# Kernel optimization log

Measured on AMD Instinct MI355X. Metric: run time of the kernel, lower is better.

Reference implementation:

```python
import jax, jax.numpy as jnp
import numpy as np

N = 8192
F_IN = 256
F_OUT = 128
NEG = -9.0e15

def setup_inputs() -> dict:
    key = jax.random.key(0)
    k1, k2, k3, k4 = jax.random.split(key, 4)
    x = jax.random.normal(k1, (N, F_IN), dtype=jnp.float32)
    adj = jax.random.randint(k2, (N, N), 0, 2, dtype=jnp.int32)
    # xavier-uniform-ish scales
    W = jax.random.normal(k3, (F_IN, F_OUT), dtype=jnp.float32) * (1.414 / np.sqrt(F_IN))
    a = jax.random.normal(k4, (2 * F_OUT, 1), dtype=jnp.float32) * (1.414 / np.sqrt(F_OUT))
    return {"x": x, "adj": adj, "W": W, "a": a}

def reference(x, adj, W, a):
    # h_i = W^T x_i  -> [N, F_OUT]
    h = x @ W
    # torch builds atom_trans[i,j] = concat(h_i, h_j); e[i,j] = leakyrelu(a1.h_i + a2.h_j)
    a1 = a[:F_OUT, 0]   # [F_OUT]
    a2 = a[F_OUT:, 0]   # [F_OUT]
    s1 = h @ a1         # [N]
    s2 = h @ a2         # [N]
    e = jax.nn.leaky_relu(s1[:, None] + s2[None, :], negative_slope=0.01)  # [N, N]
    masked = jnp.where(adj > 0, e, jnp.full_like(e, NEG))
    attention = jax.nn.softmax(masked, axis=1)
    # dropout is identity in eval mode
    h1 = attention @ h  # [N, F_OUT]
    return jax.nn.elu(h1)
```

## Files before the change

### kernel.cpp

```cpp
#include <hip/hip_runtime.h>
#include <hip/hip_bf16.h>
#include <cstdint>
#include <cstddef>

#define NN 8192
#define FIN 256
#define FO 128
#define SPLITK 8
#define JCH 1024
#define NIT 16

typedef float f32x4 __attribute__((ext_vector_type(4)));
typedef _Float16 f16x8 __attribute__((ext_vector_type(8)));

typedef __attribute__((address_space(3))) void lds_void;
typedef const __attribute__((address_space(1))) void glb_void;
__device__ __forceinline__ void gl_lds16(const void* g, void* l) {
  __builtin_amdgcn_global_load_lds((glb_void*)g, (lds_void*)l, 16, 0, 0);
}

__device__ __forceinline__ unsigned enc_f32(float f) {
  unsigned u = __float_as_uint(f);
  return (u & 0x80000000u) ? ~u : (u | 0x80000000u);
}
__device__ __forceinline__ float dec_f32(unsigned u) {
  unsigned b = (u & 0x80000000u) ? (u ^ 0x80000000u) : ~u;
  return __uint_as_float(b);
}

__global__ void k1_xw(const float* __restrict__ x, const float* __restrict__ W,
                      float* __restrict__ h, unsigned* __restrict__ enc) {
  __shared__ float xs[32 * 66];
  __shared__ float Ws[64 * 128];
  int t = threadIdx.x;
  int r0 = blockIdx.x * 32;
  if (blockIdx.x == 0 && t == 0) *enc = 0u;
  int r = t & 31, cg = t >> 5;
  float acc[16];
#pragma unroll
  for (int i = 0; i < 16; ++i) acc[i] = 0.f;
  for (int ko = 0; ko < 4; ++ko) {
    __syncthreads();
    {
      int rr = t >> 3, kc = (t & 7) * 8;
      const float2* src = (const float2*)(x + (size_t)(r0 + rr) * FIN + ko * 64 + kc);
      float2* dst = (float2*)&xs[rr * 66 + kc];
#pragma unroll
      for (int q = 0; q < 4; ++q) dst[q] = src[q];
    }
    {
      int kk = t >> 2, q = t & 3;
      const float4* src = (const float4*)(W + (size_t)(ko * 64 + kk) * FO + q * 32);
      float4* dst = (float4*)&Ws[kk * 128 + q * 32];
#pragma unroll
      for (int i = 0; i < 8; ++i) dst[i] = src[i];
    }
    __syncthreads();
#pragma unroll 8
    for (int kk = 0; kk < 64; ++kk) {
      float xv = xs[r * 66 + kk];
      const float4* wr = (const float4*)&Ws[kk * 128 + cg * 16];
      float4 w0 = wr[0], w1 = wr[1], w2 = wr[2], w3 = wr[3];
      acc[0]  = fmaf(xv, w0.x, acc[0]);  acc[1]  = fmaf(xv, w0.y, acc[1]);
      acc[2]  = fmaf(xv, w0.z, acc[2]);  acc[3]  = fmaf(xv, w0.w, acc[3]);
      acc[4]  = fmaf(xv, w1.x, acc[4]);  acc[5]  = fmaf(xv, w1.y, acc[5]);
      acc[6]  = fmaf(xv, w1.z, acc[6]);  acc[7]  = fmaf(xv, w1.w, acc[7]);
      acc[8]  = fmaf(xv, w2.x, acc[8]);  acc[9]  = fmaf(xv, w2.y, acc[9]);
      acc[10] = fmaf(xv, w2.z, acc[10]); acc[11] = fmaf(xv, w2.w, acc[11]);
      acc[12] = fmaf(xv, w3.x, acc[12]); acc[13] = fmaf(xv, w3.y, acc[13]);
      acc[14] = fmaf(xv, w3.z, acc[14]); acc[15] = fmaf(xv, w3.w, acc[15]);
    }
  }
  float* hp = h + (size_t)(r0 + r) * FO + cg * 16;
#pragma unroll
  for (int i = 0; i < 4; ++i)
    ((float4*)hp)[i] = make_float4(acc[4 * i], acc[4 * i + 1], acc[4 * i + 2], acc[4 * i + 3]);
}

__global__ void k2_prep(const float* __restrict__ h, const float* __restrict__ a,
                        _Float16* __restrict__ hT,
                        float* __restrict__ s1, float* __restrict__ s2,
                        unsigned* __restrict__ enc) {
  __shared__ float ht[64 * 129];
  int t = threadIdx.x;
  int r0 = blockIdx.x * 64;
  {
    int rr = t >> 2, q = t & 3;
    const float4* src = (const float4*)(h + (size_t)(r0 + rr) * FO + q * 32);
    float* dst = &ht[rr * 129 + q * 32];
#pragma unroll
    for (int i = 0; i < 8; ++i) {
      float4 v = src[i];
      dst[4 * i + 0] = v.x; dst[4 * i + 1] = v.y;
      dst[4 * i + 2] = v.z; dst[4 * i + 3] = v.w;
    }
  }
  __syncthreads();
  {
    int c = t >> 1, half = t & 1;
    alignas(16) _Float16 buf[32];
#pragma unroll
    for (int i = 0; i < 32; ++i) buf[i] = (_Float16)ht[(half * 32 + i) * 129 + c];
    int4* d = (int4*)(hT + (size_t)c * NN + r0 + half * 32);
#pragma unroll
    for (int i = 0; i < 4; ++i) d[i] = ((const int4*)buf)[i];
  }
  if (t < 64) {
    int row = r0 + t;
    float v1 = 0.f, v2 = 0.f;
#pragma unroll 16
    for (int c = 0; c < FO; ++c) {
      float hv = ht[t * 129 + c];
      v1 = fmaf(hv, a[c], v1);
      v2 = fmaf(hv, a[FO + c], v2);
    }
    s1[row] = v1; s2[row] = v2;
    float m = v2;
#pragma unroll
    for (int off = 1; off < 64; off <<= 1) m = fmaxf(m, __shfl_xor(m, off));
    if (t == 0) atomicMax(enc, enc_f32(m));
  }
}

__device__ __forceinline__ _Float16 wel(unsigned av, float s2v, float s1v, float mv, float& sum) {
  float tt = s1v + s2v;
  tt = fmaxf(tt, 0.01f * tt);
  float wf = av ? __expf(tt - mv) : 0.f;
  _Float16 wh = (_Float16)wf;
  sum += (float)wh;
  return wh;
}

#define K4BODY(CR, NR, BUF, JC, PF, LAST)                                        \
  {                                                                              \
    if (PF) {                                                                    \
      stage(BUF ^ 1, (JC) + 64);                                                 \
      _Pragma("unroll")                                                          \
      for (int rr = 0; rr < 16; ++rr)                                            \
        NR[rr] = abase[(size_t)rr * NN + (JC) + 64];                             \
    }                                                                            \
    __builtin_amdgcn_sched_barrier(0);                                           \
    unsigned mlo = 0u, mhi = 0u;                                                 \
    _Pragma("unroll")                                                            \
    for (int rr = 0; rr < 16; ++rr) {                                            \
      unsigned long long br = __ballot(CR[rr] > 0);                              \
      bool sel = (l15 == rr);                                                    \
      mlo = sel ? (unsigned)br : mlo;                                            \
      mhi = sel ? (unsigned)(br >> 32) : mhi;                                    \
    }                                                                            \
    _Pragma("unroll")                                                            \
    for (int ks = 0; ks < 2; ++ks) {                                             \
      unsigned mm = ks ? mhi : mlo;                                              \
      unsigned byt = (mm >> (kgrp << 3)) & 0xffu;                                \
      int jloc = ((JC) - jbeg) + ks * 32 + kgrp * 8;                             \
      f32x4 sa = *(const f32x4*)&s2l[jloc];                                      \
      f32x4 sb = *(const f32x4*)&s2l[jloc + 4];                                  \
      f16x8 af;                                                                  \
      af[0] = wel(byt & 1u,   sa[0], s10, m0, sum0);                             \
      af[1] = wel(byt & 2u,   sa[1], s10, m0, sum0);                             \
      af[2] = wel(byt & 4u,   sa[2], s10, m0, sum0);                             \
      af[3] = wel(byt & 8u,   sa[3], s10, m0, sum0);                             \
      af[4] = wel(byt & 16u,  sb[0], s10, m0, sum0);                             \
      af[5] = wel(byt & 32u,  sb[1], s10, m0, sum0);                             \
      af[6] = wel(byt & 64u,  sb[2], s10, m0, sum0);                             \
      af[7] = wel(byt & 128u, sb[3], s10, m0, sum0);                             \
      _Pragma("unroll")                                                          \
      for (int cf = 0; cf < 8; ++cf) {                                           \
        f16x8 bfr = *(const f16x8*)&tile[BUF][(cf * 16 + l15) * 64 +             \
                       ((ks * 32 + kgrp * 8) ^ (l7 * 8))];                       \
        acc[cf] = __builtin_amdgcn_mfma_f32_16x16x32_f16(af, bfr, acc[cf], 0, 0, 0); \
      }                                                                          \
    }                                                                            \
    __builtin_amdgcn_sched_barrier(0);                                           \
    if (!(LAST)) {                                                               \
      asm volatile("s_waitcnt vmcnt(16)" ::: "memory");                          \
      __builtin_amdgcn_s_barrier();                                              \
      __builtin_amdgcn_sched_barrier(0);                                         \
    }                                                                            \
  }

__global__ void __launch_bounds__(256, 4) k4_main(
    const int* __restrict__ adj, const float* __restrict__ s1g,
    const float* __restrict__ s2g, const unsigned* __restrict__ enc,
    const _Float16* __restrict__ hT,
    float* __restrict__ num_p, float* __restrict__ den_p) {
  __shared__ _Float16 tile[2][128 * 64];
  __shared__ float s2l[JCH];
  int t = threadIdx.x;
  int l = t & 63, wv = t >> 6;
  int l15 = l & 15, kgrp = l >> 4;
  int l7 = l15 & 7;
  int split = blockIdx.x;
  int r0 = blockIdx.y * 64;
  int jbeg = split * JCH;
  int row = r0 + wv * 16 + l15;

  float c2 = dec_f32(*enc);
  float s10 = s1g[row];
  float m0 = s10 + c2; m0 = fmaxf(m0, 0.01f * m0);

  f32x4 acc[8];
#pragma unroll
  for (int cf = 0; cf < 8; ++cf) acc[cf] = (f32x4){0.f, 0.f, 0.f, 0.f};
  float sum0 = 0.f;
  const int* abase = adj + (size_t)(r0 + wv * 16) * NN + l;

  auto stage = [&](int b, int jg) {
    const _Float16* g0 = hT + (size_t)(wv * 32 + (l >> 3)) * NN + jg +
                         (((l & 7) ^ (l >> 3)) * 8);
    _Float16* base = &tile[b][(wv * 32) * 64];
    gl_lds16(g0, base);
    gl_lds16(g0 + (size_t)8 * NN, base + 8 * 64);
    gl_lds16(g0 + (size_t)16 * NN, base + 16 * 64);
    gl_lds16(g0 + (size_t)24 * NN, base + 24 * 64);
  };

  int ra[16], rb[16];
  stage(0, jbeg);
  *(float4*)&s2l[t * 4] = *(const float4*)(s2g + jbeg + t * 4);
#pragma unroll
  for (int rr = 0; rr < 16; ++rr) ra[rr] = abase[(size_t)rr * NN + jbeg];
  __syncthreads();

#pragma unroll 1
  for (int tI = 0; tI < NIT; tI += 2) {
    int jc = jbeg + tI * 64;
    K4BODY(ra, rb, 0, jc, true, false);
    K4BODY(rb, ra, 1, jc + 64, (tI + 2 < NIT), (tI + 2 >= NIT));
  }

  sum0 += __shfl_xor(sum0, 16);
  sum0 += __shfl_xor(sum0, 32);
  size_t sbase = (size_t)split * NN;
  if (l < 16) den_p[sbase + r0 + wv * 16 + l] = sum0;
#pragma unroll
  for (int cf = 0; cf < 8; ++cf) {
#pragma unroll
    for (int i = 0; i < 4; ++i) {
      int orow = r0 + wv * 16 + kgrp * 4 + i;
      int ocol = cf * 16 + l15;
      num_p[(sbase + orow) * (size_t)FO + ocol] = acc[cf][i];
    }
  }
}

__global__ void k5_fin(const float* __restrict__ num_p, const float* __restrict__ den_p,
                       float* __restrict__ out) {
  int idx = blockIdx.x * 256 + threadIdx.x;
  int row = idx >> 7;
  float num = 0.f, den = 0.f;
#pragma unroll
  for (int s = 0; s < SPLITK; ++s) {
    num += num_p[(size_t)s * (NN * FO) + idx];
    den += den_p[(size_t)s * NN + row];
  }
  float v = num / den;
  out[idx] = v > 0.f ? v : expm1f(v);
}

extern "C" void kernel_launch(void* const* d_in, const int* in_sizes, int n_in,
                              void* d_out, int out_size, void* d_ws, size_t ws_size,
                              hipStream_t stream) {
  const float* x   = (const float*)d_in[0];
  const int*   adj = (const int*)d_in[1];
  const float* W   = (const float*)d_in[2];
  const float* a   = (const float*)d_in[3];
  float* out = (float*)d_out;
  char* ws = (char*)d_ws;

  float*     h     = (float*)ws;
  _Float16*  hT    = (_Float16*)(ws + ((size_t)4 << 20));
  float*     s1    = (float*)(ws + ((size_t)6 << 20));
  float*     s2    = (float*)(ws + ((size_t)6 << 20) + (32u << 10));
  unsigned*  enc   = (unsigned*)(ws + ((size_t)6 << 20) + (64u << 10));
  float*     den_p = (float*)(ws + ((size_t)6 << 20) + (128u << 10));
  float*     num_p = (float*)(ws + ((size_t)7 << 20));

  k1_xw<<<dim3(256), dim3(256), 0, stream>>>(x, W, h, enc);
  k2_prep<<<dim3(128), dim3(256), 0, stream>>>(h, a, hT, s1, s2, enc);
  k4_main<<<dim3(SPLITK, 128), dim3(256), 0, stream>>>(adj, s1, s2, enc, hT,
                                                       num_p, den_p);
  k5_fin<<<dim3((NN * FO) / 256), dim3(256), 0, stream>>>(num_p, den_p, out);
}
```

Baseline: 114.9 us.

## Load adjacency as int2 pairs over 128-column superblocks with split even/odd ballots

Each lane now loads two adjacent adjacency ints (int2) per row, so one set of 16 loads covers 128 columns instead of 64. Ballots are split into even and odd masks, and the weight construction interleaves bits from the two masks. The main loop is restructured into superblocks of two 64-column MFMA phases, with hT staging and barriers rearranged. This halves the number of adjacency load instructions and ballot rounds per column. In exchange it adds scheduling complexity and different vmcnt accounting.

```diff
diff --git a/kernel.cpp b/kernel.cpp
--- a/kernel.cpp
+++ b/kernel.cpp
@@ -8,7 +8,7 @@
 #define FO 128
 #define SPLITK 8
 #define JCH 1024
-#define NIT 16
+#define NSB 8
 
 typedef float f32x4 __attribute__((ext_vector_type(4)));
 typedef _Float16 f16x8 __attribute__((ext_vector_type(8)));
@@ -131,51 +131,30 @@
   return wh;
 }
 
-#define K4BODY(CR, NR, BUF, JC, PF, LAST)                                        \
+#define K4COMPUTE(MEV, MOD, BUFI, SBASE)                                         \
   {                                                                              \
-    if (PF) {                                                                    \
-      stage(BUF ^ 1, (JC) + 64);                                                 \
-      _Pragma("unroll")                                                          \
-      for (int rr = 0; rr < 16; ++rr)                                            \
-        NR[rr] = abase[(size_t)rr * NN + (JC) + 64];                             \
-    }                                                                            \
-    __builtin_amdgcn_sched_barrier(0);                                           \
-    unsigned mlo = 0u, mhi = 0u;                                                 \
-    _Pragma("unroll")                                                            \
-    for (int rr = 0; rr < 16; ++rr) {                                            \
-      unsigned long long br = __ballot(CR[rr] > 0);                              \
-      bool sel = (l15 == rr);                                                    \
-      mlo = sel ? (unsigned)br : mlo;                                            \
-      mhi = sel ? (unsigned)(br >> 32) : mhi;                                    \
-    }                                                                            \
     _Pragma("unroll")                                                            \
     for (int ks = 0; ks < 2; ++ks) {                                             \
-      unsigned mm = ks ? mhi : mlo;                                              \
-      unsigned byt = (mm >> (kgrp << 3)) & 0xffu;                                \
-      int jloc = ((JC) - jbeg) + ks * 32 + kgrp * 8;                             \
+      unsigned ne = ((MEV) >> (ks * 16 + kgrp * 4)) & 0xfu;                      \
+      unsigned no = ((MOD) >> (ks * 16 + kgrp * 4)) & 0xfu;                      \
+      int jloc = (SBASE) + ks * 32 + kgrp * 8;                                   \
       f32x4 sa = *(const f32x4*)&s2l[jloc];                                      \
       f32x4 sb = *(const f32x4*)&s2l[jloc + 4];                                  \
       f16x8 af;                                                                  \
-      af[0] = wel(byt & 1u,   sa[0], s10, m0, sum0);                             \
-      af[1] = wel(byt & 2u,   sa[1], s10, m0, sum0);                             \
-      af[2] = wel(byt & 4u,   sa[2], s10, m0, sum0);                             \
-      af[3] = wel(byt & 8u,   sa[3], s10, m0, sum0);                             \
-      af[4] = wel(byt & 16u,  sb[0], s10, m0, sum0);                             \
-      af[5] = wel(byt & 32u,  sb[1], s10, m0, sum0);                             \
-      af[6] = wel(byt & 64u,  sb[2], s10, m0, sum0);                             \
-      af[7] = wel(byt & 128u, sb[3], s10, m0, sum0);                             \
+      af[0] = wel(ne & 1u, sa[0], s10, m0, sum0);                                \
+      af[1] = wel(no & 1u, sa[1], s10, m0, sum0);                                \
+      af[2] = wel(ne & 2u, sa[2], s10, m0, sum0);                                \
+      af[3] = wel(no & 2u, sa[3], s10, m0, sum0);                                \
+      af[4] = wel(ne & 4u, sb[0], s10, m0, sum0);                                \
+      af[5] = wel(no & 4u, sb[1], s10, m0, sum0);                                \
+      af[6] = wel(ne & 8u, sb[2], s10, m0, sum0);                                \
+      af[7] = wel(no & 8u, sb[3], s10, m0, sum0);                                \
       _Pragma("unroll")                                                          \
       for (int cf = 0; cf < 8; ++cf) {                                           \
-        f16x8 bfr = *(const f16x8*)&tile[BUF][(cf * 16 + l15) * 64 +             \
+        f16x8 bfr = *(const f16x8*)&tile[BUFI][(cf * 16 + l15) * 64 +            \
                        ((ks * 32 + kgrp * 8) ^ (l7 * 8))];                       \
         acc[cf] = __builtin_amdgcn_mfma_f32_16x16x32_f16(af, bfr, acc[cf], 0, 0, 0); \
       }                                                                          \
-    }                                                                            \
-    __builtin_amdgcn_sched_barrier(0);                                           \
-    if (!(LAST)) {                                                               \
-      asm volatile("s_waitcnt vmcnt(16)" ::: "memory");                          \
-      __builtin_amdgcn_s_barrier();                                              \
-      __builtin_amdgcn_sched_barrier(0);                                         \
     }                                                                            \
   }
 
@@ -203,7 +182,7 @@
 #pragma unroll
   for (int cf = 0; cf < 8; ++cf) acc[cf] = (f32x4){0.f, 0.f, 0.f, 0.f};
   float sum0 = 0.f;
-  const int* abase = adj + (size_t)(r0 + wv * 16) * NN + l;
+  const int* abase = adj + (size_t)(r0 + wv * 16) * NN + 2 * l;
 
   auto stage = [&](int b, int jg) {
     const _Float16* g0 = hT + (size_t)(wv * 32 + (l >> 3)) * NN + jg +
@@ -215,31 +194,72 @@
     gl_lds16(g0 + (size_t)24 * NN, base + 24 * 64);
   };
 
-  int ra[16], rb[16];
+  int2 S[16];
+#define LOADSET2(J)                                                              \
+  _Pragma("unroll")                                                              \
+  for (int rr = 0; rr < 16; ++rr)                                                \
+    S[rr] = *(const int2*)(abase + (size_t)rr * NN + (J));
+
+  unsigned mev_lo, mev_hi, mod_lo, mod_hi;
+#define BALLOTROUTE()                                                            \
+  {                                                                              \
+    mev_lo = 0u; mev_hi = 0u; mod_lo = 0u; mod_hi = 0u;                          \
+    _Pragma("unroll")                                                            \
+    for (int rr = 0; rr < 16; ++rr) {                                            \
+      unsigned long long be = __ballot(S[rr].x > 0);                             \
+      unsigned long long bo = __ballot(S[rr].y > 0);                             \
+      bool sel = (l15 == rr);                                                    \
+      mev_lo = sel ? (unsigned)be : mev_lo;                                      \
+      mev_hi = sel ? (unsigned)(be >> 32) : mev_hi;                              \
+      mod_lo = sel ? (unsigned)bo : mod_lo;                                      \
+      mod_hi = sel ? (unsigned)(bo >> 32) : mod_hi;                              \
+    }                                                                            \
+  }
+
   stage(0, jbeg);
+  LOADSET2(jbeg)
   *(float4*)&s2l[t * 4] = *(const float4*)(s2g + jbeg + t * 4);
-#pragma unroll
-  for (int rr = 0; rr < 16; ++rr) ra[rr] = abase[(size_t)rr * NN + jbeg];
-  __syncthreads();
+  asm volatile("s_waitcnt vmcnt(0) lgkmcnt(0)" ::: "memory");
+  __builtin_amdgcn_s_barrier();
+  __builtin_amdgcn_sched_barrier(0);
+  BALLOTROUTE()
 
 #pragma unroll 1
-  for (int tI = 0; tI < NIT; tI += 2) {
-    int jc = jbeg + tI * 64;
-    K4BODY(ra, rb, 0, jc, true, false);
-    K4BODY(rb, ra, 1, jc + 64, (tI + 2 < NIT), (tI + 2 >= NIT));
+  for (int sb = 0; sb < NSB; ++sb) {
+    int sjb = jbeg + sb * 128;
+    int sbase = sb * 128;
+    stage(1, sjb + 64);
+    if (sb + 1 < NSB) { LOADSET2(sjb + 128) }
+    __builtin_amdgcn_sched_barrier(0);
+    K4COMPUTE(mev_lo, mod_lo, 0, sbase)
+    __builtin_amdgcn_sched_barrier(0);
+    if (sb + 1 < NSB) asm volatile("s_waitcnt vmcnt(16)" ::: "memory");
+    else              asm volatile("s_waitcnt vmcnt(0)" ::: "memory");
+    __builtin_amdgcn_s_barrier();
+    __builtin_amdgcn_sched_barrier(0);
+    if (sb + 1 < NSB) stage(0, sjb + 128);
+    __builtin_amdgcn_sched_barrier(0);
+    K4COMPUTE(mev_hi, mod_hi, 1, sbase + 64)
+    __builtin_amdgcn_sched_barrier(0);
+    if (sb + 1 < NSB) {
+      asm volatile("s_waitcnt vmcnt(0)" ::: "memory");
+      __builtin_amdgcn_s_barrier();
+      __builtin_amdgcn_sched_barrier(0);
+      BALLOTROUTE()
+    }
   }
 
   sum0 += __shfl_xor(sum0, 16);
   sum0 += __shfl_xor(sum0, 32);
-  size_t sbase = (size_t)split * NN;
-  if (l < 16) den_p[sbase + r0 + wv * 16 + l] = sum0;
+  size_t sbase2 = (size_t)split * NN;
+  if (l < 16) den_p[sbase2 + r0 + wv * 16 + l] = sum0;
 #pragma unroll
   for (int cf = 0; cf < 8; ++cf) {
 #pragma unroll
     for (int i = 0; i < 4; ++i) {
       int orow = r0 + wv * 16 + kgrp * 4 + i;
       int ocol = cf * 16 + l15;
-      num_p[(sbase + orow) * (size_t)FO + ocol] = acc[cf][i];
+      num_p[(sbase2 + orow) * (size_t)FO + ocol] = acc[cf][i];
     }
   }
 }
```

After: 120.2 us. +4.6%, slower.

## Warp-specialize attention kernel with producer waves building adjacency bitmasks in LDS

Applied to the files above, without the earlier changes.

Adds two producer waves per block that load the int32 adjacency with 16-byte vector loads, ballot it into 64-bit masks and store them in shared memory. The four consumer waves stage h tiles and run the MFMA softmax-weighted accumulation, reading the precomputed masks. The aim is to take the adjacency loads and ballots off the MFMA waves' critical path and widen the adj loads. The cost is 384-thread blocks with lower occupancy, extra LDS for the masks, and a per-step barrier shared by both roles.

```diff
diff --git a/kernel.cpp b/kernel.cpp
--- a/kernel.cpp
+++ b/kernel.cpp
@@ -8,10 +8,10 @@
 #define FO 128
 #define SPLITK 8
 #define JCH 1024
-#define NIT 16
 
 typedef float f32x4 __attribute__((ext_vector_type(4)));
 typedef _Float16 f16x8 __attribute__((ext_vector_type(8)));
+typedef unsigned long long ull;
 
 typedef __attribute__((address_space(3))) void lds_void;
 typedef const __attribute__((address_space(1))) void glb_void;
@@ -131,79 +131,116 @@
   return wh;
 }
 
-#define K4BODY(CR, NR, BUF, JC, PF, LAST)                                        \
+#define PLOAD(SET, T)                                                            \
+  if ((T) < 8) {                                                                 \
+    int wl_ = ((T) >> 2) + 2, sub_ = (T) & 3;                                    \
+    const int* pb = adj + (size_t)(r0 + p32 + sub_ * 8) * NN + jbeg +            \
+                    wl_ * 256 + 4 * l;                                           \
+    _Pragma("unroll")                                                            \
+    for (int rr = 0; rr < 8; ++rr)                                               \
+      SET[rr] = *(const int4*)(pb + (size_t)rr * NN);                            \
+  }
+
+#define PBALLOT(SET, T)                                                          \
+  if ((T) >= 1 && (T) <= 8) {                                                    \
+    int wl_ = (((T) - 1) >> 2) + 2, sub_ = ((T) - 1) & 3;                        \
+    if ((T) < 8) asm volatile("s_waitcnt vmcnt(8)" ::: "memory");                \
+    else         asm volatile("s_waitcnt vmcnt(0)" ::: "memory");                \
+    _Pragma("unroll")                                                            \
+    for (int rr = 0; rr < 8; ++rr) {                                             \
+      ull b0 = __ballot(SET[rr].x > 0);                                          \
+      ull b1 = __ballot(SET[rr].y > 0);                                          \
+      ull b2 = __ballot(SET[rr].z > 0);                                          \
+      ull b3 = __ballot(SET[rr].w > 0);                                          \
+      if (l == 0) {                                                              \
+        int row_ = p32 + sub_ * 8 + rr;                                          \
+        masksL[row_][wl_ * 4 + 0] = b0;                                          \
+        masksL[row_][wl_ * 4 + 1] = b1;                                          \
+        masksL[row_][wl_ * 4 + 2] = b2;                                          \
+        masksL[row_][wl_ * 4 + 3] = b3;                                          \
+      }                                                                          \
+    }                                                                            \
+  }
+
+#define CONSUME(BUFI, T)                                                         \
   {                                                                              \
-    if (PF) {                                                                    \
-      stage(BUF ^ 1, (JC) + 64);                                                 \
-      _Pragma("unroll")                                                          \
-      for (int rr = 0; rr < 16; ++rr)                                            \
-        NR[rr] = abase[(size_t)rr * NN + (JC) + 64];                             \
-    }                                                                            \
-    __builtin_amdgcn_sched_barrier(0);                                           \
-    unsigned mlo = 0u, mhi = 0u;                                                 \
-    _Pragma("unroll")                                                            \
-    for (int rr = 0; rr < 16; ++rr) {                                            \
-      unsigned long long br = __ballot(CR[rr] > 0);                              \
-      bool sel = (l15 == rr);                                                    \
-      mlo = sel ? (unsigned)br : mlo;                                            \
-      mhi = sel ? (unsigned)(br >> 32) : mhi;                                    \
-    }                                                                            \
+    int win_ = (T) >> 2, sub_ = (T) & 3;                                         \
+    const ull* mrow = &masksL[(wv << 4) + l15][win_ << 2];                       \
+    ull w0 = mrow[0] >> sh2, w1 = mrow[1] >> sh2,                                \
+        w2 = mrow[2] >> sh2, w3 = mrow[3] >> sh2;                                \
     _Pragma("unroll")                                                            \
     for (int ks = 0; ks < 2; ++ks) {                                             \
-      unsigned mm = ks ? mhi : mlo;                                              \
-      unsigned byt = (mm >> (kgrp << 3)) & 0xffu;                                \
-      int jloc = ((JC) - jbeg) + ks * 32 + kgrp * 8;                             \
+      int SH = sub_ * 16 + ks * 8;                                               \
+      unsigned b0 = (unsigned)(w0 >> SH);                                        \
+      unsigned b1 = (unsigned)(w1 >> SH);                                        \
+      unsigned b2 = (unsigned)(w2 >> SH);                                        \
+      unsigned b3 = (unsigned)(w3 >> SH);                                        \
+      int jloc = (T) * 64 + ks * 32 + kgrp * 8;                                  \
       f32x4 sa = *(const f32x4*)&s2l[jloc];                                      \
       f32x4 sb = *(const f32x4*)&s2l[jloc + 4];                                  \
       f16x8 af;                                                                  \
-      af[0] = wel(byt & 1u,   sa[0], s10, m0, sum0);                             \
-      af[1] = wel(byt & 2u,   sa[1], s10, m0, sum0);                             \
-      af[2] = wel(byt & 4u,   sa[2], s10, m0, sum0);                             \
-      af[3] = wel(byt & 8u,   sa[3], s10, m0, sum0);                             \
-      af[4] = wel(byt & 16u,  sb[0], s10, m0, sum0);                             \
-      af[5] = wel(byt & 32u,  sb[1], s10, m0, sum0);                             \
-      af[6] = wel(byt & 64u,  sb[2], s10, m0, sum0);                             \
-      af[7] = wel(byt & 128u, sb[3], s10, m0, sum0);                             \
+      af[0] = wel(b0 & 1u, sa[0], s10, m0, sum0);                                \
+      af[1] = wel(b1 & 1u, sa[1], s10, m0, sum0);                                \
+      af[2] = wel(b2 & 1u, sa[2], s10, m0, sum0);                                \
+      af[3] = wel(b3 & 1u, sa[3], s10, m0, sum0);                                \
+      af[4] = wel(b0 & 2u, sb[0], s10, m0, sum0);                                \
+      af[5] = wel(b1 & 2u, sb[1], s10, m0, sum0);                                \
+      af[6] = wel(b2 & 2u, sb[2], s10, m0, sum0);                                \
+      af[7] = wel(b3 & 2u, sb[3], s10, m0, sum0);                                \
       _Pragma("unroll")                                                          \
       for (int cf = 0; cf < 8; ++cf) {                                           \
-        f16x8 bfr = *(const f16x8*)&tile[BUF][(cf * 16 + l15) * 64 +             \
+        f16x8 bfr = *(const f16x8*)&tile[(BUFI)][(cf * 16 + l15) * 64 +          \
                        ((ks * 32 + kgrp * 8) ^ (l7 * 8))];                       \
         acc[cf] = __builtin_amdgcn_mfma_f32_16x16x32_f16(af, bfr, acc[cf], 0, 0, 0); \
       }                                                                          \
     }                                                                            \
+  }
+
+#define BODYALL(T, LSET, BSET)                                                   \
+  {                                                                              \
+    if (wv < 4) {                                                                \
+      if ((T) < 15) stage(((T) + 1) & 1, jbeg + ((T) + 1) * 64);                 \
+      CONSUME((T) & 1, T)                                                        \
+    } else {                                                                     \
+      PLOAD(LSET, T)                                                             \
+      PBALLOT(BSET, T)                                                           \
+    }                                                                            \
     __builtin_amdgcn_sched_barrier(0);                                           \
-    if (!(LAST)) {                                                               \
-      asm volatile("s_waitcnt vmcnt(16)" ::: "memory");                          \
+    if ((T) < 15) {                                                              \
+      if (wv < 4) asm volatile("s_waitcnt vmcnt(0)" ::: "memory");               \
+      else        asm volatile("s_waitcnt lgkmcnt(0)" ::: "memory");             \
       __builtin_amdgcn_s_barrier();                                              \
       __builtin_amdgcn_sched_barrier(0);                                         \
     }                                                                            \
   }
 
-__global__ void __launch_bounds__(256, 4) k4_main(
+__global__ void __launch_bounds__(384, 3) k4_main(
     const int* __restrict__ adj, const float* __restrict__ s1g,
     const float* __restrict__ s2g, const unsigned* __restrict__ enc,
     const _Float16* __restrict__ hT,
     float* __restrict__ num_p, float* __restrict__ den_p) {
   __shared__ _Float16 tile[2][128 * 64];
   __shared__ float s2l[JCH];
+  __shared__ ull masksL[64][16];
   int t = threadIdx.x;
   int l = t & 63, wv = t >> 6;
   int l15 = l & 15, kgrp = l >> 4;
   int l7 = l15 & 7;
+  int sh2 = kgrp * 2;
   int split = blockIdx.x;
   int r0 = blockIdx.y * 64;
   int jbeg = split * JCH;
-  int row = r0 + wv * 16 + l15;
-
+  int p32 = (wv - 4) * 32;
+
+  int crow = r0 + (wv & 3) * 16 + l15;
   float c2 = dec_f32(*enc);
-  float s10 = s1g[row];
+  float s10 = s1g[crow];
   float m0 = s10 + c2; m0 = fmaxf(m0, 0.01f * m0);
 
   f32x4 acc[8];
 #pragma unroll
   for (int cf = 0; cf < 8; ++cf) acc[cf] = (f32x4){0.f, 0.f, 0.f, 0.f};
   float sum0 = 0.f;
-  const int* abase = adj + (size_t)(r0 + wv * 16) * NN + l;
 
   auto stage = [&](int b, int jg) {
     const _Float16* g0 = hT + (size_t)(wv * 32 + (l >> 3)) * NN + jg +
@@ -215,31 +252,62 @@
     gl_lds16(g0 + (size_t)24 * NN, base + 24 * 64);
   };
 
-  int ra[16], rb[16];
-  stage(0, jbeg);
-  *(float4*)&s2l[t * 4] = *(const float4*)(s2g + jbeg + t * 4);
-#pragma unroll
-  for (int rr = 0; rr < 16; ++rr) ra[rr] = abase[(size_t)rr * NN + jbeg];
-  __syncthreads();
-
+  int4 Sa[8], Sb[8];
+
+  if (wv < 4) {
+    stage(0, jbeg);
+    asm volatile("s_waitcnt vmcnt(0)" ::: "memory");
+  } else {
 #pragma unroll 1
-  for (int tI = 0; tI < NIT; tI += 2) {
-    int jc = jbeg + tI * 64;
-    K4BODY(ra, rb, 0, jc, true, false);
-    K4BODY(rb, ra, 1, jc + 64, (tI + 2 < NIT), (tI + 2 >= NIT));
-  }
-
-  sum0 += __shfl_xor(sum0, 16);
-  sum0 += __shfl_xor(sum0, 32);
-  size_t sbase = (size_t)split * NN;
-  if (l < 16) den_p[sbase + r0 + wv * 16 + l] = sum0;
-#pragma unroll
-  for (int cf = 0; cf < 8; ++cf) {
-#pragma unroll
-    for (int i = 0; i < 4; ++i) {
-      int orow = r0 + wv * 16 + kgrp * 4 + i;
-      int ocol = cf * 16 + l15;
-      num_p[(sbase + orow) * (size_t)FO + ocol] = acc[cf][i];
+    for (int ch = 0; ch < 4; ++ch) {
+      int win = ch >> 1, rh = (ch & 1) * 16;
+      int4 T[16];
+#pragma unroll
+      for (int rr = 0; rr < 16; ++rr)
+        T[rr] = *(const int4*)(adj + (size_t)(r0 + p32 + rh + rr) * NN +
+                               jbeg + win * 256 + 4 * l);
+      asm volatile("s_waitcnt vmcnt(0)" ::: "memory");
+#pragma unroll
+      for (int rr = 0; rr < 16; ++rr) {
+        ull b0 = __ballot(T[rr].x > 0);
+        ull b1 = __ballot(T[rr].y > 0);
+        ull b2 = __ballot(T[rr].z > 0);
+        ull b3 = __ballot(T[rr].w > 0);
+        if (l == 0) {
+          int row_ = p32 + rh + rr;
+          masksL[row_][win * 4 + 0] = b0;
+          masksL[row_][win * 4 + 1] = b1;
+          masksL[row_][win * 4 + 2] = b2;
+          masksL[row_][win * 4 + 3] = b3;
+        }
+      }
+    }
+    asm volatile("s_waitcnt lgkmcnt(0)" ::: "memory");
+  }
+  if (t < 256) *(float4*)&s2l[t * 4] = *(const float4*)(s2g + jbeg + t * 4);
+  asm volatile("s_waitcnt lgkmcnt(0)" ::: "memory");
+  __builtin_amdgcn_s_barrier();
+  __builtin_amdgcn_sched_barrier(0);
+
+#pragma unroll 1
+  for (int tI = 0; tI < 16; tI += 2) {
+    BODYALL(tI, Sa, Sb)
+    BODYALL(tI + 1, Sb, Sa)
+  }
+
+  if (wv < 4) {
+    sum0 += __shfl_xor(sum0, 16);
+    sum0 += __shfl_xor(sum0, 32);
+    size_t sbase = (size_t)split * NN;
+    if (l < 16) den_p[sbase + r0 + wv * 16 + l] = sum0;
+#pragma unroll
+    for (int cf = 0; cf < 8; ++cf) {
+#pragma unroll
+      for (int i = 0; i < 4; ++i) {
+        int orow = r0 + wv * 16 + kgrp * 4 + i;
+        int ocol = cf * 16 + l15;
+        num_p[(sbase + orow) * (size_t)FO + ocol] = acc[cf][i];
+      }
     }
   }
 }
@@ -278,7 +346,7 @@
 
   k1_xw<<<dim3(256), dim3(256), 0, stream>>>(x, W, h, enc);
   k2_prep<<<dim3(128), dim3(256), 0, stream>>>(h, a, hT, s1, s2, enc);
-  k4_main<<<dim3(SPLITK, 128), dim3(256), 0, stream>>>(adj, s1, s2, enc, hT,
+  k4_main<<<dim3(SPLITK, 128), dim3(384), 0, stream>>>(adj, s1, s2, enc, hT,
                                                        num_p, den_p);
   k5_fin<<<dim3((NN * FO) / 256), dim3(256), 0, stream>>>(num_p, den_p, out);
 }
```

Measured after the change: 159.7 us. 1.39x slower.

## Load adjacency as int4 windows with rebuilt ballot masks and fp16 partial sums

Applied to the files above, without the earlier changes.

The adjacency mask is now read as 16-byte int4 vectors over 256-column windows instead of scalar ints per 64-column step. Ballots are rebuilt into 64-bit masks that are staggered across a fully unrolled 16-step schedule with explicit vmcnt waits. This is meant to cut the number of global load instructions and in-flight registers on the dominant adj stream. It also stores the split-K numerator partials as fp16 instead of fp32, halving that write and read traffic at some accuracy risk. The bit-to-column mapping now interleaves four columns per lane and must match the s2 and tile ordering exactly.

```diff
diff --git a/kernel.cpp b/kernel.cpp
--- a/kernel.cpp
+++ b/kernel.cpp
@@ -8,10 +8,10 @@
 #define FO 128
 #define SPLITK 8
 #define JCH 1024
-#define NIT 16
 
 typedef float f32x4 __attribute__((ext_vector_type(4)));
 typedef _Float16 f16x8 __attribute__((ext_vector_type(8)));
+typedef unsigned long long ull;
 
 typedef __attribute__((address_space(3))) void lds_void;
 typedef const __attribute__((address_space(1))) void glb_void;
@@ -131,49 +131,67 @@
   return wh;
 }
 
-#define K4BODY(CR, NR, BUF, JC, PF, LAST)                                        \
+#define LOAD4(SET, WIN, P)                                                       \
+  _Pragma("unroll")                                                              \
+  for (int rr = 0; rr < 4; ++rr)                                                 \
+    SET[rr] = *(const int4*)(abase + (size_t)(4 * (P) + rr) * NN +               \
+                             jbeg + (WIN) * 256);
+
+#define BAL4(SET, P, M0, M1, M2, M3)                                             \
+  _Pragma("unroll")                                                              \
+  for (int rr = 0; rr < 4; ++rr) {                                               \
+    ull b0 = __ballot(SET[rr].x > 0);                                            \
+    ull b1 = __ballot(SET[rr].y > 0);                                            \
+    ull b2 = __ballot(SET[rr].z > 0);                                            \
+    ull b3 = __ballot(SET[rr].w > 0);                                            \
+    bool sel = (l15 == 4 * (P) + rr);                                            \
+    M0 = sel ? (b0 >> sh2) : M0;                                                 \
+    M1 = sel ? (b1 >> sh2) : M1;                                                 \
+    M2 = sel ? (b2 >> sh2) : M2;                                                 \
+    M3 = sel ? (b3 >> sh2) : M3;                                                 \
+  }
+
+#define CONS(M0, M1, M2, M3, T)                                                  \
   {                                                                              \
-    if (PF) {                                                                    \
-      stage(BUF ^ 1, (JC) + 64);                                                 \
-      _Pragma("unroll")                                                          \
-      for (int rr = 0; rr < 16; ++rr)                                            \
-        NR[rr] = abase[(size_t)rr * NN + (JC) + 64];                             \
-    }                                                                            \
-    __builtin_amdgcn_sched_barrier(0);                                           \
-    unsigned mlo = 0u, mhi = 0u;                                                 \
-    _Pragma("unroll")                                                            \
-    for (int rr = 0; rr < 16; ++rr) {                                            \
-      unsigned long long br = __ballot(CR[rr] > 0);                              \
-      bool sel = (l15 == rr);                                                    \
-      mlo = sel ? (unsigned)br : mlo;                                            \
-      mhi = sel ? (unsigned)(br >> 32) : mhi;                                    \
-    }                                                                            \
     _Pragma("unroll")                                                            \
     for (int ks = 0; ks < 2; ++ks) {                                             \
-      unsigned mm = ks ? mhi : mlo;                                              \
-      unsigned byt = (mm >> (kgrp << 3)) & 0xffu;                                \
-      int jloc = ((JC) - jbeg) + ks * 32 + kgrp * 8;                             \
+      int SH = ((T) & 3) * 16 + ks * 8;                                          \
+      unsigned c0 = (unsigned)((M0) >> SH);                                      \
+      unsigned c1 = (unsigned)((M1) >> SH);                                      \
+      unsigned c2 = (unsigned)((M2) >> SH);                                      \
+      unsigned c3 = (unsigned)((M3) >> SH);                                      \
+      int jloc = (T) * 64 + ks * 32 + kgrp * 8;                                  \
       f32x4 sa = *(const f32x4*)&s2l[jloc];                                      \
       f32x4 sb = *(const f32x4*)&s2l[jloc + 4];                                  \
       f16x8 af;                                                                  \
-      af[0] = wel(byt & 1u,   sa[0], s10, m0, sum0);                             \
-      af[1] = wel(byt & 2u,   sa[1], s10, m0, sum0);                             \
-      af[2] = wel(byt & 4u,   sa[2], s10, m0, sum0);                             \
-      af[3] = wel(byt & 8u,   sa[3], s10, m0, sum0);                             \
-      af[4] = wel(byt & 16u,  sb[0], s10, m0, sum0);                             \
-      af[5] = wel(byt & 32u,  sb[1], s10, m0, sum0);                             \
-      af[6] = wel(byt & 64u,  sb[2], s10, m0, sum0);                             \
-      af[7] = wel(byt & 128u, sb[3], s10, m0, sum0);                             \
+      af[0] = wel(c0 & 1u, sa[0], s10, mx0, sum0);                               \
+      af[1] = wel(c1 & 1u, sa[1], s10, mx0, sum0);                               \
+      af[2] = wel(c2 & 1u, sa[2], s10, mx0, sum0);                               \
+      af[3] = wel(c3 & 1u, sa[3], s10, mx0, sum0);                               \
+      af[4] = wel(c0 & 2u, sb[0], s10, mx0, sum0);                               \
+      af[5] = wel(c1 & 2u, sb[1], s10, mx0, sum0);                               \
+      af[6] = wel(c2 & 2u, sb[2], s10, mx0, sum0);                               \
+      af[7] = wel(c3 & 2u, sb[3], s10, mx0, sum0);                               \
       _Pragma("unroll")                                                          \
       for (int cf = 0; cf < 8; ++cf) {                                           \
-        f16x8 bfr = *(const f16x8*)&tile[BUF][(cf * 16 + l15) * 64 +             \
+        f16x8 bfr = *(const f16x8*)&tile[(T) & 1][(cf * 16 + l15) * 64 +         \
                        ((ks * 32 + kgrp * 8) ^ (l7 * 8))];                       \
         acc[cf] = __builtin_amdgcn_mfma_f32_16x16x32_f16(af, bfr, acc[cf], 0, 0, 0); \
       }                                                                          \
     }                                                                            \
+  }
+
+#define BODY(T, DOL, LSET, WIN, PL, DOB, BSET, PB,                               \
+             CM0, CM1, CM2, CM3, BM0, BM1, BM2, BM3, VMS)                        \
+  {                                                                              \
+    if ((T) < 15) stage(((T) + 1) & 1, jbeg + ((T) + 1) * 64);                   \
+    if (DOL) { LOAD4(LSET, WIN, PL) }                                            \
+    if (DOB) { BAL4(BSET, PB, BM0, BM1, BM2, BM3) }                              \
     __builtin_amdgcn_sched_barrier(0);                                           \
-    if (!(LAST)) {                                                               \
-      asm volatile("s_waitcnt vmcnt(16)" ::: "memory");                          \
+    CONS(CM0, CM1, CM2, CM3, T)                                                  \
+    __builtin_amdgcn_sched_barrier(0);                                           \
+    if ((T) < 15) {                                                              \
+      asm volatile("s_waitcnt vmcnt(" VMS ")" ::: "memory");                     \
       __builtin_amdgcn_s_barrier();                                              \
       __builtin_amdgcn_sched_barrier(0);                                         \
     }                                                                            \
@@ -183,13 +201,14 @@
     const int* __restrict__ adj, const float* __restrict__ s1g,
     const float* __restrict__ s2g, const unsigned* __restrict__ enc,
     const _Float16* __restrict__ hT,
-    float* __restrict__ num_p, float* __restrict__ den_p) {
+    _Float16* __restrict__ num_p, float* __restrict__ den_p) {
   __shared__ _Float16 tile[2][128 * 64];
   __shared__ float s2l[JCH];
   int t = threadIdx.x;
   int l = t & 63, wv = t >> 6;
   int l15 = l & 15, kgrp = l >> 4;
   int l7 = l15 & 7;
+  int sh2 = kgrp * 2;
   int split = blockIdx.x;
   int r0 = blockIdx.y * 64;
   int jbeg = split * JCH;
@@ -197,13 +216,13 @@
 
   float c2 = dec_f32(*enc);
   float s10 = s1g[row];
-  float m0 = s10 + c2; m0 = fmaxf(m0, 0.01f * m0);
+  float mx0 = s10 + c2; mx0 = fmaxf(mx0, 0.01f * mx0);
 
   f32x4 acc[8];
 #pragma unroll
   for (int cf = 0; cf < 8; ++cf) acc[cf] = (f32x4){0.f, 0.f, 0.f, 0.f};
   float sum0 = 0.f;
-  const int* abase = adj + (size_t)(r0 + wv * 16) * NN + l;
+  const int* abase = adj + (size_t)(r0 + wv * 16) * NN + 4 * l;
 
   auto stage = [&](int b, int jg) {
     const _Float16* g0 = hT + (size_t)(wv * 32 + (l >> 3)) * NN + jg +
@@ -215,19 +234,41 @@
     gl_lds16(g0 + (size_t)24 * NN, base + 24 * 64);
   };
 
-  int ra[16], rb[16];
+  int4 Sa[4], Sb[4];
+  ull Ma0, Ma1, Ma2, Ma3;
+  ull Mb0, Mb1, Mb2, Mb3;
+  Ma0 = Ma1 = Ma2 = Ma3 = 0; Mb0 = Mb1 = Mb2 = Mb3 = 0;
+
   stage(0, jbeg);
+  LOAD4(Sa, 0, 0)
+  LOAD4(Sb, 0, 1)
   *(float4*)&s2l[t * 4] = *(const float4*)(s2g + jbeg + t * 4);
-#pragma unroll
-  for (int rr = 0; rr < 16; ++rr) ra[rr] = abase[(size_t)rr * NN + jbeg];
-  __syncthreads();
-
-#pragma unroll 1
-  for (int tI = 0; tI < NIT; tI += 2) {
-    int jc = jbeg + tI * 64;
-    K4BODY(ra, rb, 0, jc, true, false);
-    K4BODY(rb, ra, 1, jc + 64, (tI + 2 < NIT), (tI + 2 >= NIT));
-  }
+  BAL4(Sa, 0, Ma0, Ma1, Ma2, Ma3)
+  LOAD4(Sa, 0, 2)
+  BAL4(Sb, 1, Ma0, Ma1, Ma2, Ma3)
+  LOAD4(Sb, 0, 3)
+  BAL4(Sa, 2, Ma0, Ma1, Ma2, Ma3)
+  BAL4(Sb, 3, Ma0, Ma1, Ma2, Ma3)
+  asm volatile("s_waitcnt vmcnt(0) lgkmcnt(0)" ::: "memory");
+  __builtin_amdgcn_s_barrier();
+  __builtin_amdgcn_sched_barrier(0);
+
+  BODY(0,  1, Sa, 1, 0,  0, Sb, 0, Ma0, Ma1, Ma2, Ma3, Mb0, Mb1, Mb2, Mb3, "4")
+  BODY(1,  1, Sb, 1, 1,  1, Sa, 0, Ma0, Ma1, Ma2, Ma3, Mb0, Mb1, Mb2, Mb3, "4")
+  BODY(2,  1, Sa, 1, 2,  1, Sb, 1, Ma0, Ma1, Ma2, Ma3, Mb0, Mb1, Mb2, Mb3, "4")
+  BODY(3,  1, Sb, 1, 3,  1, Sa, 2, Ma0, Ma1, Ma2, Ma3, Mb0, Mb1, Mb2, Mb3, "4")
+  BODY(4,  1, Sa, 2, 0,  1, Sb, 3, Mb0, Mb1, Mb2, Mb3, Mb0, Mb1, Mb2, Mb3, "4")
+  BODY(5,  1, Sb, 2, 1,  1, Sa, 0, Mb0, Mb1, Mb2, Mb3, Ma0, Ma1, Ma2, Ma3, "4")
+  BODY(6,  1, Sa, 2, 2,  1, Sb, 1, Mb0, Mb1, Mb2, Mb3, Ma0, Ma1, Ma2, Ma3, "4")
+  BODY(7,  1, Sb, 2, 3,  1, Sa, 2, Mb0, Mb1, Mb2, Mb3, Ma0, Ma1, Ma2, Ma3, "4")
+  BODY(8,  1, Sa, 3, 0,  1, Sb, 3, Ma0, Ma1, Ma2, Ma3, Ma0, Ma1, Ma2, Ma3, "4")
+  BODY(9,  1, Sb, 3, 1,  1, Sa, 0, Ma0, Ma1, Ma2, Ma3, Mb0, Mb1, Mb2, Mb3, "4")
+  BODY(10, 1, Sa, 3, 2,  1, Sb, 1, Ma0, Ma1, Ma2, Ma3, Mb0, Mb1, Mb2, Mb3, "4")
+  BODY(11, 1, Sb, 3, 3,  1, Sa, 2, Ma0, Ma1, Ma2, Ma3, Mb0, Mb1, Mb2, Mb3, "4")
+  BODY(12, 0, Sa, 3, 0,  1, Sb, 3, Mb0, Mb1, Mb2, Mb3, Mb0, Mb1, Mb2, Mb3, "0")
+  BODY(13, 0, Sa, 3, 0,  0, Sb, 0, Mb0, Mb1, Mb2, Mb3, Mb0, Mb1, Mb2, Mb3, "0")
+  BODY(14, 0, Sa, 3, 0,  0, Sb, 0, Mb0, Mb1, Mb2, Mb3, Mb0, Mb1, Mb2, Mb3, "0")
+  BODY(15, 0, Sa, 3, 0,  0, Sb, 0, Mb0, Mb1, Mb2, Mb3, Mb0, Mb1, Mb2, Mb3, "0")
 
   sum0 += __shfl_xor(sum0, 16);
   sum0 += __shfl_xor(sum0, 32);
@@ -239,19 +280,19 @@
     for (int i = 0; i < 4; ++i) {
       int orow = r0 + wv * 16 + kgrp * 4 + i;
       int ocol = cf * 16 + l15;
-      num_p[(sbase + orow) * (size_t)FO + ocol] = acc[cf][i];
-    }
-  }
-}
-
-__global__ void k5_fin(const float* __restrict__ num_p, const float* __restrict__ den_p,
-                       float* __restrict__ out) {
+      num_p[(sbase + orow) * (size_t)FO + ocol] = (_Float16)acc[cf][i];
+    }
+  }
+}
+
+__global__ void k5_fin(const _Float16* __restrict__ num_p,
+                       const float* __restrict__ den_p, float* __restrict__ out) {
   int idx = blockIdx.x * 256 + threadIdx.x;
   int row = idx >> 7;
   float num = 0.f, den = 0.f;
 #pragma unroll
   for (int s = 0; s < SPLITK; ++s) {
-    num += num_p[(size_t)s * (NN * FO) + idx];
+    num += (float)num_p[(size_t)s * (NN * FO) + idx];
     den += den_p[(size_t)s * NN + row];
   }
   float v = num / den;
@@ -274,7 +315,7 @@
   float*     s2    = (float*)(ws + ((size_t)6 << 20) + (32u << 10));
   unsigned*  enc   = (unsigned*)(ws + ((size_t)6 << 20) + (64u << 10));
   float*     den_p = (float*)(ws + ((size_t)6 << 20) + (128u << 10));
-  float*     num_p = (float*)(ws + ((size_t)7 << 20));
+  _Float16*  num_p = (_Float16*)(ws + ((size_t)7 << 20));
 
   k1_xw<<<dim3(256), dim3(256), 0, stream>>>(x, W, h, enc);
   k2_prep<<<dim3(128), dim3(256), 0, stream>>>(h, a, hT, s1, s2, enc);
```

Result: slower. 149.9 us (+30.4%).
